# Kernel optimization log

Hardware: AMD Instinct MI355X
Metric: run time of the kernel (lower is better)

Reference implementation:

```python
import jax, jax.numpy as jnp
import numpy as np


def setup_inputs() -> dict:
    key = jax.random.key(0)
    k1, k2 = jax.random.split(key)
    B, Lq, Lc, D = 16, 512, 2048, 1024
    question = jax.random.normal(k1, (B, Lq, D), dtype=jnp.float32)
    context = jax.random.normal(k2, (B, Lc, D), dtype=jnp.float32)
    return {"question": question, "context": context}


def reference(question, context):
    # e = context @ question^T : [B, Lc, Lq]  (unscaled)
    e = jnp.einsum("bcd,bqd->bcq", context, question)
    attn = jax.nn.softmax(e, axis=-1)
    # attention_output = attn @ question : [B, Lc, D]
    attn_out = jnp.einsum("bcq,bqd->bcd", attn, question)
    # concat along feature dim -> [B, Lc, 2D]; dropout is identity at eval
    return jnp.concatenate([context, attn_out], axis=-1)
```

## Files before the change

### kernel.cpp

```cpp
#include <hip/hip_runtime.h>

#define GAS __attribute__((address_space(1)))
#define LAS __attribute__((address_space(3)))

typedef __attribute__((ext_vector_type(8))) _Float16 half8;
typedef __attribute__((ext_vector_type(4))) float floatx4;
typedef __attribute__((ext_vector_type(4))) unsigned short ushort4v;

static constexpr int B_  = 16;
static constexpr int LQ  = 512;
static constexpr int LC  = 2048;
static constexpr int D_  = 1024;
static constexpr int DO  = 2048;
static constexpr int MT  = 64;
static constexpr int BUFSZ = 36864;

__device__ __forceinline__ void gl2lds16(const void* g, void* l) {
  __builtin_amdgcn_global_load_lds((const GAS unsigned int*)g,
                                   (LAS unsigned int*)l, 16, 0, 0);
}

__device__ __forceinline__ unsigned short f2h(float f) {
  return __builtin_bit_cast(unsigned short, (_Float16)f);
}

__global__ void qprep_kernel(const float* __restrict__ q,
                             unsigned short* __restrict__ qh,
                             unsigned short* __restrict__ qt) {
  __shared__ unsigned short t[32][33];
  const int b = blockIdx.z, d0 = blockIdx.x * 32, q0 = blockIdx.y * 32;
  const float* src = q + (size_t)b * LQ * D_;
  unsigned short* dq = qh + (size_t)b * LQ * D_;
  unsigned short* dt = qt + (size_t)b * D_ * LQ;
  for (int i = threadIdx.y; i < 32; i += 8) {
    const unsigned short h = f2h(src[(size_t)(q0 + i) * D_ + d0 + threadIdx.x]);
    dq[(size_t)(q0 + i) * D_ + d0 + threadIdx.x] = h;
    t[i][threadIdx.x] = h;
  }
  __syncthreads();
  for (int i = threadIdx.y; i < 32; i += 8)
    dt[(size_t)(d0 + i) * LQ + q0 + threadIdx.x] = t[threadIdx.x][i];
}

__global__ void cprep_kernel(const float* __restrict__ src,
                             unsigned short* __restrict__ dst,
                             float* __restrict__ out) {
  const int nrows = B_ * LC;
  for (int row = blockIdx.x; row < nrows; row += gridDim.x) {
    const float4 v = ((const float4*)(src + (size_t)row * D_))[threadIdx.x];
    ushort4v h;
    h.x = f2h(v.x); h.y = f2h(v.y); h.z = f2h(v.z); h.w = f2h(v.w);
    ((ushort4v*)(dst + (size_t)row * D_))[threadIdx.x] = h;
    ((float4*)(out + (size_t)row * DO))[threadIdx.x] = v;
  }
}

__launch_bounds__(512, 4)
__global__ void attn_main(const unsigned short* __restrict__ qg,
                          const unsigned short* __restrict__ cg,
                          const unsigned short* __restrict__ qtg,
                          unsigned short* __restrict__ pg,
                          float* __restrict__ og) {
  __shared__ __align__(16) char smem[2 * BUFSZ + 2048 + 256];
  float* redf    = (float*)(smem + 2 * BUFSZ);
  float* rowstat = (float*)(smem + 2 * BUFSZ + 2048);

  const int tid  = threadIdx.x;
  const int wave = tid >> 6;
  const int lane = tid & 63;
  const int l15  = lane & 15;
  const int quad = lane >> 4;
  const int q8   = quad * 8;

  const int b    = blockIdx.x & 15;
  const int tile = blockIdx.x >> 4;
  const int c0   = tile * MT;

  const unsigned short* Q  = qg  + (size_t)b * LQ * D_;
  const unsigned short* C  = cg  + (size_t)b * LC * D_;
  const unsigned short* QT = qtg + (size_t)b * D_ * LQ;
  unsigned short*       P  = pg  + (size_t)b * LC * LQ;
  float*                O  = og  + (size_t)b * LC * DO;

  floatx4 acc[4][4];

  auto stage1 = [&](int it, char* buf) {
    const int k0 = it * 32;
#pragma unroll
    for (int j = 0; j < 5; ++j) {
      const int bb = wave + j * 8;
      if (bb < 32) {
        gl2lds16(Q + (size_t)(bb * 16 + l15) * D_ + k0 + q8, buf + bb * 1024);
      } else if (bb < 36) {
        const int mt = bb - 32;
        gl2lds16(C + (size_t)(c0 + mt * 16 + l15) * D_ + k0 + q8,
                 buf + 32768 + mt * 1024);
      }
    }
  };

  auto stage2 = [&](int nh, int itq, char* buf) {
    const int kq = itq * 32;
#pragma unroll
    for (int j = 0; j < 5; ++j) {
      const int bb = wave + j * 8;
      if (bb < 32) {
        gl2lds16(QT + (size_t)(nh * 512 + bb * 16 + l15) * LQ + kq + q8,
                 buf + bb * 1024);
      } else if (bb < 36) {
        const int mt = bb - 32;
        gl2lds16(P + (size_t)(c0 + mt * 16 + l15) * LQ + kq + q8,
                 buf + 32768 + mt * 1024);
      }
    }
  };

  auto compute = [&](const char* buf) {
    half8 af[4], bf[4];
#pragma unroll
    for (int mt = 0; mt < 4; ++mt)
      af[mt] = *(const half8*)(buf + 32768 + mt * 1024 + lane * 16);
#pragma unroll
    for (int nt = 0; nt < 4; ++nt)
      bf[nt] = *(const half8*)(buf + (wave * 4 + nt) * 1024 + lane * 16);
#pragma unroll
    for (int mt = 0; mt < 4; ++mt)
#pragma unroll
      for (int nt = 0; nt < 4; ++nt)
        acc[mt][nt] = __builtin_amdgcn_mfma_f32_16x16x32_f16(
            af[mt], bf[nt], acc[mt][nt], 0, 0, 0);
  };

  auto wait_prev = [&]() {
    if (wave < 4) asm volatile("s_waitcnt vmcnt(5)" ::: "memory");
    else          asm volatile("s_waitcnt vmcnt(4)" ::: "memory");
  };

#pragma unroll
  for (int i = 0; i < 4; ++i)
#pragma unroll
    for (int j = 0; j < 4; ++j) acc[i][j] = floatx4{0.f, 0.f, 0.f, 0.f};

  stage1(0, smem);
  int cur = 0;
#pragma unroll 1
  for (int it = 0; it < 32; ++it) {
    if (it + 1 < 32) {
      stage1(it + 1, smem + (cur ^ 1) * BUFSZ);
      wait_prev();
    } else {
      asm volatile("s_waitcnt vmcnt(0)" ::: "memory");
    }
    __builtin_amdgcn_s_barrier();
    __builtin_amdgcn_sched_barrier(0);
    compute(smem + cur * BUFSZ);
    asm volatile("" ::: "memory");
    __builtin_amdgcn_s_barrier();
    cur ^= 1;
  }

#pragma unroll
  for (int mt = 0; mt < 4; ++mt)
#pragma unroll
    for (int r = 0; r < 4; ++r) {
      float m = fmaxf(fmaxf(acc[mt][0][r], acc[mt][1][r]),
                      fmaxf(acc[mt][2][r], acc[mt][3][r]));
      m = fmaxf(m, __shfl_xor(m, 1, 64));
      m = fmaxf(m, __shfl_xor(m, 2, 64));
      m = fmaxf(m, __shfl_xor(m, 4, 64));
      m = fmaxf(m, __shfl_xor(m, 8, 64));
      if (l15 == 0) redf[wave * 64 + mt * 16 + quad * 4 + r] = m;
    }
  __syncthreads();
  if (tid < 64) {
    float m = redf[tid];
#pragma unroll
    for (int w = 1; w < 8; ++w) m = fmaxf(m, redf[w * 64 + tid]);
    rowstat[tid] = m;
  }
  __syncthreads();
#pragma unroll
  for (int mt = 0; mt < 4; ++mt)
#pragma unroll
    for (int r = 0; r < 4; ++r) {
      const float m = rowstat[mt * 16 + quad * 4 + r];
      float s = 0.f;
#pragma unroll
      for (int nt = 0; nt < 4; ++nt) {
        const float e = __expf(acc[mt][nt][r] - m);
        acc[mt][nt][r] = e;
        s += e;
      }
      s += __shfl_xor(s, 1, 64);
      s += __shfl_xor(s, 2, 64);
      s += __shfl_xor(s, 4, 64);
      s += __shfl_xor(s, 8, 64);
      if (l15 == 0) redf[wave * 64 + mt * 16 + quad * 4 + r] = s;
    }
  __syncthreads();
  if (tid < 64) {
    float s = 0.f;
#pragma unroll
    for (int w = 0; w < 8; ++w) s += redf[w * 64 + tid];
    rowstat[tid] = 1.0f / s;
  }
  __syncthreads();
#pragma unroll
  for (int mt = 0; mt < 4; ++mt)
#pragma unroll
    for (int r = 0; r < 4; ++r) {
      const float inv = rowstat[mt * 16 + quad * 4 + r];
      const size_t rowoff =
          (size_t)(c0 + mt * 16 + quad * 4 + r) * LQ + wave * 64 + l15;
#pragma unroll
      for (int nt = 0; nt < 4; ++nt)
        P[rowoff + nt * 16] = f2h(acc[mt][nt][r] * inv);
    }
  asm volatile("s_waitcnt vmcnt(0)" ::: "memory");
  __syncthreads();

#pragma unroll 1
  for (int nh = 0; nh < 2; ++nh) {
#pragma unroll
    for (int i = 0; i < 4; ++i)
#pragma unroll
      for (int j = 0; j < 4; ++j) acc[i][j] = floatx4{0.f, 0.f, 0.f, 0.f};
    stage2(nh, 0, smem);
    cur = 0;
#pragma unroll 1
    for (int itq = 0; itq < 16; ++itq) {
      if (itq + 1 < 16) {
        stage2(nh, itq + 1, smem + (cur ^ 1) * BUFSZ);
        wait_prev();
      } else {
        asm volatile("s_waitcnt vmcnt(0)" ::: "memory");
      }
      __builtin_amdgcn_s_barrier();
      __builtin_amdgcn_sched_barrier(0);
      compute(smem + cur * BUFSZ);
      asm volatile("" ::: "memory");
      __builtin_amdgcn_s_barrier();
      cur ^= 1;
    }
#pragma unroll
    for (int mt = 0; mt < 4; ++mt)
#pragma unroll
      for (int r = 0; r < 4; ++r) {
        const size_t rowoff = (size_t)(c0 + mt * 16 + quad * 4 + r) * DO +
                              D_ + nh * 512 + wave * 64 + l15;
#pragma unroll
        for (int nt = 0; nt < 4; ++nt)
          O[rowoff + nt * 16] = acc[mt][nt][r];
      }
  }
}

extern "C" void kernel_launch(void* const* d_in, const int* in_sizes, int n_in,
                              void* d_out, int out_size, void* d_ws, size_t ws_size,
                              hipStream_t stream) {
  (void)in_sizes; (void)n_in; (void)out_size; (void)ws_size;
  const float* q = (const float*)d_in[0];
  const float* c = (const float*)d_in[1];
  float* out = (float*)d_out;
  unsigned short* qh  = (unsigned short*)d_ws;
  unsigned short* ch  = qh  + (size_t)B_ * LQ * D_;
  unsigned short* qth = ch  + (size_t)B_ * LC * D_;
  unsigned short* p   = qth + (size_t)B_ * D_ * LQ;
  qprep_kernel<<<dim3(D_ / 32, LQ / 32, B_), dim3(32, 8), 0, stream>>>(q, qh, qth);
  cprep_kernel<<<2048, 256, 0, stream>>>(c, ch, out);
  attn_main<<<dim3(B_ * (LC / MT)), dim3(512), 0, stream>>>(qh, ch, qth, p, out);
}
```

Baseline: 567.0 us.

## Deepen attention GEMM pipeline to four LDS stages and flatten second GEMM

Replaces the double-buffered LDS pipeline in both GEMM phases with a four-slot ring that keeps three tile loads in flight, issuing each new load after the barrier. The two output-half loops of the second GEMM become one flattened 32-step pipeline, so prefetch continues across the half boundary instead of draining. MFMA blocks are wrapped in s_setprio and launch bounds drop to one block per SIMD group. The LDS footprint roughly doubles, which cuts resident blocks per CU and may expose more latency than the deeper prefetch hides. The mid-loop output stores also add to the vmcnt counter the hand-written waits rely on.

```diff
diff --git a/kernel.cpp b/kernel.cpp
--- a/kernel.cpp
+++ b/kernel.cpp
@@ -23,6 +23,12 @@
 __device__ __forceinline__ unsigned short f2h(float f) {
   return __builtin_bit_cast(unsigned short, (_Float16)f);
 }
+
+#define WAITV(a, b)                                                        \
+  do {                                                                     \
+    if (wave < 4) asm volatile("s_waitcnt vmcnt(" #a ")" ::: "memory");    \
+    else          asm volatile("s_waitcnt vmcnt(" #b ")" ::: "memory");    \
+  } while (0)
 
 __global__ void qprep_kernel(const float* __restrict__ q,
                              unsigned short* __restrict__ qh,
@@ -55,15 +61,15 @@
   }
 }
 
-__launch_bounds__(512, 4)
+__launch_bounds__(512, 1)
 __global__ void attn_main(const unsigned short* __restrict__ qg,
                           const unsigned short* __restrict__ cg,
                           const unsigned short* __restrict__ qtg,
                           unsigned short* __restrict__ pg,
                           float* __restrict__ og) {
-  __shared__ __align__(16) char smem[2 * BUFSZ + 2048 + 256];
-  float* redf    = (float*)(smem + 2 * BUFSZ);
-  float* rowstat = (float*)(smem + 2 * BUFSZ + 2048);
+  __shared__ __align__(16) char smem[4 * BUFSZ + 2048 + 256];
+  float* redf    = (float*)(smem + 4 * BUFSZ);
+  float* rowstat = (float*)(smem + 4 * BUFSZ + 2048);
 
   const int tid  = threadIdx.x;
   const int wave = tid >> 6;
@@ -99,8 +105,9 @@
     }
   };
 
-  auto stage2 = [&](int nh, int itq, char* buf) {
-    const int kq = itq * 32;
+  auto stage2 = [&](int u, char* buf) {
+    const int nh = u >> 4;
+    const int kq = (u & 15) * 32;
 #pragma unroll
     for (int j = 0; j < 5; ++j) {
       const int bb = wave + j * 8;
@@ -123,40 +130,35 @@
 #pragma unroll
     for (int nt = 0; nt < 4; ++nt)
       bf[nt] = *(const half8*)(buf + (wave * 4 + nt) * 1024 + lane * 16);
+    __builtin_amdgcn_s_setprio(1);
 #pragma unroll
     for (int mt = 0; mt < 4; ++mt)
 #pragma unroll
       for (int nt = 0; nt < 4; ++nt)
         acc[mt][nt] = __builtin_amdgcn_mfma_f32_16x16x32_f16(
             af[mt], bf[nt], acc[mt][nt], 0, 0, 0);
+    __builtin_amdgcn_s_setprio(0);
   };
 
-  auto wait_prev = [&]() {
-    if (wave < 4) asm volatile("s_waitcnt vmcnt(5)" ::: "memory");
-    else          asm volatile("s_waitcnt vmcnt(4)" ::: "memory");
-  };
-
 #pragma unroll
   for (int i = 0; i < 4; ++i)
 #pragma unroll
     for (int j = 0; j < 4; ++j) acc[i][j] = floatx4{0.f, 0.f, 0.f, 0.f};
 
   stage1(0, smem);
-  int cur = 0;
+  stage1(1, smem + BUFSZ);
+  stage1(2, smem + 2 * BUFSZ);
 #pragma unroll 1
-  for (int it = 0; it < 32; ++it) {
-    if (it + 1 < 32) {
-      stage1(it + 1, smem + (cur ^ 1) * BUFSZ);
-      wait_prev();
-    } else {
-      asm volatile("s_waitcnt vmcnt(0)" ::: "memory");
-    }
+  for (int t = 0; t < 32; ++t) {
+    if (t <= 29)      WAITV(10, 8);
+    else if (t == 30) WAITV(5, 4);
+    else asm volatile("s_waitcnt vmcnt(0)" ::: "memory");
     __builtin_amdgcn_s_barrier();
     __builtin_amdgcn_sched_barrier(0);
-    compute(smem + cur * BUFSZ);
+    if (t + 3 < 32) stage1(t + 3, smem + ((t + 3) & 3) * BUFSZ);
+    compute(smem + (t & 3) * BUFSZ);
     asm volatile("" ::: "memory");
     __builtin_amdgcn_s_barrier();
-    cur ^= 1;
   }
 
 #pragma unroll
@@ -219,39 +221,39 @@
   asm volatile("s_waitcnt vmcnt(0)" ::: "memory");
   __syncthreads();
 
+  stage2(0, smem);
+  stage2(1, smem + BUFSZ);
+  stage2(2, smem + 2 * BUFSZ);
 #pragma unroll 1
-  for (int nh = 0; nh < 2; ++nh) {
-#pragma unroll
-    for (int i = 0; i < 4; ++i)
-#pragma unroll
-      for (int j = 0; j < 4; ++j) acc[i][j] = floatx4{0.f, 0.f, 0.f, 0.f};
-    stage2(nh, 0, smem);
-    cur = 0;
-#pragma unroll 1
-    for (int itq = 0; itq < 16; ++itq) {
-      if (itq + 1 < 16) {
-        stage2(nh, itq + 1, smem + (cur ^ 1) * BUFSZ);
-        wait_prev();
-      } else {
-        asm volatile("s_waitcnt vmcnt(0)" ::: "memory");
-      }
-      __builtin_amdgcn_s_barrier();
-      __builtin_amdgcn_sched_barrier(0);
-      compute(smem + cur * BUFSZ);
-      asm volatile("" ::: "memory");
-      __builtin_amdgcn_s_barrier();
-      cur ^= 1;
-    }
-#pragma unroll
-    for (int mt = 0; mt < 4; ++mt)
-#pragma unroll
-      for (int r = 0; r < 4; ++r) {
-        const size_t rowoff = (size_t)(c0 + mt * 16 + quad * 4 + r) * DO +
-                              D_ + nh * 512 + wave * 64 + l15;
-#pragma unroll
-        for (int nt = 0; nt < 4; ++nt)
-          O[rowoff + nt * 16] = acc[mt][nt][r];
-      }
+  for (int u = 0; u < 32; ++u) {
+    if ((u & 15) == 0) {
+#pragma unroll
+      for (int i = 0; i < 4; ++i)
+#pragma unroll
+        for (int j = 0; j < 4; ++j) acc[i][j] = floatx4{0.f, 0.f, 0.f, 0.f};
+    }
+    if (u <= 29)      WAITV(10, 8);
+    else if (u == 30) WAITV(5, 4);
+    else asm volatile("s_waitcnt vmcnt(0)" ::: "memory");
+    __builtin_amdgcn_s_barrier();
+    __builtin_amdgcn_sched_barrier(0);
+    if (u + 3 < 32) stage2(u + 3, smem + ((u + 3) & 3) * BUFSZ);
+    compute(smem + (u & 3) * BUFSZ);
+    asm volatile("" ::: "memory");
+    __builtin_amdgcn_s_barrier();
+    if ((u & 15) == 15) {
+      const int nh = u >> 4;
+#pragma unroll
+      for (int mt = 0; mt < 4; ++mt)
+#pragma unroll
+        for (int r = 0; r < 4; ++r) {
+          const size_t rowoff = (size_t)(c0 + mt * 16 + quad * 4 + r) * DO +
+                                D_ + nh * 512 + wave * 64 + l15;
+#pragma unroll
+          for (int nt = 0; nt < 4; ++nt)
+            O[rowoff + nt * 16] = acc[mt][nt][r];
+        }
+    }
   }
 }
 
```

Result: no change. 565.8 us (-0.2%).
